# Kernel tuning notes

Measured on AMD Instinct MI355X. Metric: run time of the kernel, lower is better.

## Reference

```python
import jax, jax.numpy as jnp
import numpy as np

EPS = 1e-5

def layer_norm(x, g, b):
    m = jnp.mean(x, axis=-1, keepdims=True)
    v = jnp.mean(jnp.square(x - m), axis=-1, keepdims=True)
    return (x - m) * jax.lax.rsqrt(v + EPS) * g + b

def setup_inputs() -> dict:
    key = jax.random.key(0)
    ks = jax.random.split(key, 12)
    B, N, D, C = 1, 384, 128, 128
    s_in = 1.0 / np.sqrt(D)
    s_c = 1.0 / np.sqrt(C)
    return {
        "z": jax.random.normal(ks[0], (B, N, N, D), dtype=jnp.float32),
        "mask": jnp.ones((B, N, N), dtype=jnp.float32),
        "norm_g": jnp.ones((D,), jnp.float32),
        "norm_b": jnp.zeros((D,), jnp.float32),
        "norm_out_g": jnp.ones((C,), jnp.float32),
        "norm_out_b": jnp.zeros((C,), jnp.float32),
        "Wa": jax.random.normal(ks[1], (D, C), jnp.float32) * s_in,
        "ba": jnp.zeros((C,), jnp.float32),
        "Wb": jax.random.normal(ks[2], (D, C), jnp.float32) * s_in,
        "bb": jnp.zeros((C,), jnp.float32),
        "Wga": jax.random.normal(ks[3], (D, C), jnp.float32) * s_in,
        "bga": jnp.zeros((C,), jnp.float32),
        "Wgb": jax.random.normal(ks[4], (D, C), jnp.float32) * s_in,
        "bgb": jnp.zeros((C,), jnp.float32),
        "Wo": jax.random.normal(ks[5], (C, D), jnp.float32) * s_c,
        "bo": jnp.zeros((D,), jnp.float32),
        "Wgo": jax.random.normal(ks[6], (D, D), jnp.float32) * s_in,
        "bgo": jnp.zeros((D,), jnp.float32),
    }

def reference(z, mask, norm_g, norm_b, norm_out_g, norm_out_b,
              Wa, ba, Wb, bb, Wga, bga, Wgb, bgb, Wo, bo, Wgo, bgo):
    # z: [B,N,N,D]; mask: [B,N,N]
    z_norm = layer_norm(z, norm_g, norm_b)
    left = (z_norm @ Wa + ba) * jax.nn.sigmoid(z_norm @ Wga + bga)   # [B,N,N,C]
    right = (z_norm @ Wb + bb) * jax.nn.sigmoid(z_norm @ Wgb + bgb)  # [B,N,N,C]
    m = mask[..., None]
    left = left * m
    right = right * m
    # z_out[b,i,j,c] = sum_k left[b,i,k,c] * right[b,j,k,c]
    z_out = jnp.einsum('bikc,bjkc->bijc', left, right)
    z_out = layer_norm(z_out, norm_out_g, norm_out_b)
    z_update = (z_out @ Wo + bo) * jax.nn.sigmoid(z_norm @ Wgo + bgo)
    return z_update
```

## Files before the change

kernel.cpp:

```cpp
#include <hip/hip_runtime.h>


#define NSEQ 384
#define NROW (384 * 384)

typedef __attribute__((ext_vector_type(8))) short bf16x8;
typedef __attribute__((ext_vector_type(4))) float f32x4;

__device__ __forceinline__ float sigmoidf_(float x) {
    return 1.0f / (1.0f + __expf(-x));
}
__device__ __forceinline__ unsigned short bf16_rne(float f) {
    unsigned int u = __float_as_uint(f);
    u += 0x7FFFu + ((u >> 16) & 1u);
    return (unsigned short)(u >> 16);
}
__device__ __forceinline__ float bf16_tof(unsigned short h) {
    return __uint_as_float(((unsigned int)h) << 16);
}

__global__ __launch_bounds__(256) void proj_kernel(
    const float* __restrict__ z, const float* __restrict__ mask,
    const float* __restrict__ ng, const float* __restrict__ nb,
    const float* __restrict__ Wa, const float* __restrict__ ba,
    const float* __restrict__ Wga, const float* __restrict__ bga,
    const float* __restrict__ Wb, const float* __restrict__ bb,
    const float* __restrict__ Wgb, const float* __restrict__ bgb,
    const float* __restrict__ Wgo, const float* __restrict__ bgo,
    unsigned short* __restrict__ lH, unsigned short* __restrict__ lL,
    unsigned short* __restrict__ rH, unsigned short* __restrict__ rL,
    float* __restrict__ go)
{
    __shared__ float At[128][68];
    __shared__ float Ws[128][64];
    float* Tt = &Ws[0][0];
    const int t = threadIdx.x;
    const int tx = t & 15, ty = t >> 4;
    const int row0 = blockIdx.x * 64;

#pragma unroll
    for (int it = 0; it < 8; ++it) {
        const int f = t + it * 256;
        const int r = f >> 5;
        const int c4 = (f & 31) << 2;
        const float4 v = *reinterpret_cast<const float4*>(z + (size_t)(row0 + r) * 128 + c4);
        At[c4 + 0][r] = v.x;
        At[c4 + 1][r] = v.y;
        At[c4 + 2][r] = v.z;
        At[c4 + 3][r] = v.w;
    }
    __syncthreads();

    {
        const int r = t >> 2, sub = t & 3;
        float s = 0.f, ss = 0.f;
#pragma unroll
        for (int q = 0; q < 32; ++q) {
            const float x = At[sub * 32 + q][r];
            s += x;
            ss += x * x;
        }
        s += __shfl_xor(s, 1);  ss += __shfl_xor(ss, 1);
        s += __shfl_xor(s, 2);  ss += __shfl_xor(ss, 2);
        const float m = s * (1.f / 128.f);
        const float inv = rsqrtf(ss * (1.f / 128.f) - m * m + 1e-5f);
#pragma unroll
        for (int q = 0; q < 32; ++q) {
            const int k = sub * 32 + q;
            At[k][r] = (At[k][r] - m) * inv * ng[k] + nb[k];
        }
    }

    float mk[4];
#pragma unroll
    for (int m = 0; m < 4; ++m) mk[m] = mask[row0 + ty * 4 + m];

    float accA[4][4], accG[4][4];

#define LOAD_W(Wp, h)                                                              \
    __syncthreads();                                                               \
    _Pragma("unroll")                                                              \
    for (int it = 0; it < 8; ++it) {                                               \
        const int f = t + it * 256;                                                \
        const int k = f >> 4;                                                      \
        const int c4 = (f & 15) << 2;                                              \
        *reinterpret_cast<float4*>(&Ws[k][c4]) =                                   \
            *reinterpret_cast<const float4*>((Wp) + k * 128 + (h) * 64 + c4);      \
    }                                                                              \
    __syncthreads();

#define MM(acc)                                                                    \
    _Pragma("unroll")                                                              \
    for (int m = 0; m < 4; ++m)                                                    \
        _Pragma("unroll")                                                          \
        for (int n = 0; n < 4; ++n) (acc)[m][n] = 0.f;                             \
    _Pragma("unroll 8")                                                            \
    for (int k = 0; k < 128; ++k) {                                                \
        const float4 a = *reinterpret_cast<const float4*>(&At[k][ty * 4]);         \
        const float4 b = *reinterpret_cast<const float4*>(&Ws[k][tx * 4]);         \
        const float av[4] = {a.x, a.y, a.z, a.w};                                  \
        const float bv[4] = {b.x, b.y, b.z, b.w};                                  \
        _Pragma("unroll")                                                          \
        for (int m = 0; m < 4; ++m)                                                \
            _Pragma("unroll")                                                      \
            for (int n = 0; n < 4; ++n) (acc)[m][n] = fmaf(av[m], bv[n], (acc)[m][n]); \
    }

#define STORE_T_BF(dstH, dstL, h, EXPR_X, EXPR_Y, EXPR_Z, EXPR_W)                  \
    __syncthreads();                                  \
    _Pragma("unroll")                                                              \
    for (int m = 0; m < 4; ++m) {                                                  \
        Tt[(tx * 4 + 0) * 65 + ty * 4 + m] = (EXPR_X);                             \
        Tt[(tx * 4 + 1) * 65 + ty * 4 + m] = (EXPR_Y);                             \
        Tt[(tx * 4 + 2) * 65 + ty * 4 + m] = (EXPR_Z);                             \
        Tt[(tx * 4 + 3) * 65 + ty * 4 + m] = (EXPR_W);                             \
    }                                                                              \
    __syncthreads();                                                               \
    _Pragma("unroll")                                                              \
    for (int p = 0; p < 4; ++p) {                                                  \
        const int f = t + p * 256;                                    \
        const int c = f >> 4;                                 \
        const int r4 = (f & 15) << 2;                                              \
        ushort4 hv, lv;                                                            \
        const float v0 = Tt[c * 65 + r4 + 0];                                      \
        const float v1 = Tt[c * 65 + r4 + 1];                                      \
        const float v2 = Tt[c * 65 + r4 + 2];                                      \
        const float v3 = Tt[c * 65 + r4 + 3];                                      \
        hv.x = bf16_rne(v0); lv.x = bf16_rne(v0 - bf16_tof(hv.x));                 \
        hv.y = bf16_rne(v1); lv.y = bf16_rne(v1 - bf16_tof(hv.y));                 \
        hv.z = bf16_rne(v2); lv.z = bf16_rne(v2 - bf16_tof(hv.z));                 \
        hv.w = bf16_rne(v3); lv.w = bf16_rne(v3 - bf16_tof(hv.w));                 \
        const size_t off = (size_t)((h) * 64 + c) * NROW + row0 + r4;              \
        *reinterpret_cast<ushort4*>((dstH) + off) = hv;                            \
        *reinterpret_cast<ushort4*>((dstL) + off) = lv;                            \
    }

    for (int h = 0; h < 2; ++h) {
        const int c0 = h * 64 + tx * 4;

        LOAD_W(Wa, h);  MM(accA);
        LOAD_W(Wga, h); MM(accG);
        {
            const float4 b1 = *reinterpret_cast<const float4*>(ba + c0);
            const float4 b2 = *reinterpret_cast<const float4*>(bga + c0);
            STORE_T_BF(lH, lL, h,
                (accA[m][0] + b1.x) * sigmoidf_(accG[m][0] + b2.x) * mk[m],
                (accA[m][1] + b1.y) * sigmoidf_(accG[m][1] + b2.y) * mk[m],
                (accA[m][2] + b1.z) * sigmoidf_(accG[m][2] + b2.z) * mk[m],
                (accA[m][3] + b1.w) * sigmoidf_(accG[m][3] + b2.w) * mk[m]);
        }

        LOAD_W(Wb, h);  MM(accA);
        LOAD_W(Wgb, h); MM(accG);
        {
            const float4 b1 = *reinterpret_cast<const float4*>(bb + c0);
            const float4 b2 = *reinterpret_cast<const float4*>(bgb + c0);
            STORE_T_BF(rH, rL, h,
                (accA[m][0] + b1.x) * sigmoidf_(accG[m][0] + b2.x) * mk[m],
                (accA[m][1] + b1.y) * sigmoidf_(accG[m][1] + b2.y) * mk[m],
                (accA[m][2] + b1.z) * sigmoidf_(accG[m][2] + b2.z) * mk[m],
                (accA[m][3] + b1.w) * sigmoidf_(accG[m][3] + b2.w) * mk[m]);
        }

        LOAD_W(Wgo, h); MM(accA);
        {
            const float4 b1 = *reinterpret_cast<const float4*>(bgo + c0);
#pragma unroll
            for (int m = 0; m < 4; ++m) {
                float4 o;
                o.x = sigmoidf_(accA[m][0] + b1.x);
                o.y = sigmoidf_(accA[m][1] + b1.y);
                o.z = sigmoidf_(accA[m][2] + b1.z);
                o.w = sigmoidf_(accA[m][3] + b1.w);
                *reinterpret_cast<float4*>(go + (size_t)(row0 + ty * 4 + m) * 128 + c0) = o;
            }
        }
    }
#undef LOAD_W
#undef MM
#undef STORE_T_BF
}

__global__ __launch_bounds__(256) void tri_mfma_kernel(
    const unsigned short* __restrict__ lH, const unsigned short* __restrict__ lL,
    const unsigned short* __restrict__ rH, const unsigned short* __restrict__ rL,
    float* __restrict__ zo)
{
    __shared__ unsigned short Ah[128][40];
    __shared__ unsigned short Al[128][40];
    __shared__ unsigned short Bh[128][40];
    __shared__ unsigned short Bl[128][40];

    const int t = threadIdx.x;
    const int w = t >> 6, l = t & 63;
    const int c  = blockIdx.x;
    const int i0 = blockIdx.y * 128;
    const int j0 = blockIdx.z * 128;
    const int iw = (w >> 1) * 64;
    const int jw = (w & 1) * 64;
    const int lr = l & 15;
    const int lk = (l >> 4) * 8;

    f32x4 acc[4][4];
#pragma unroll
    for (int m = 0; m < 4; ++m)
#pragma unroll
        for (int n = 0; n < 4; ++n) {
            acc[m][n][0] = 0.f; acc[m][n][1] = 0.f;
            acc[m][n][2] = 0.f; acc[m][n][3] = 0.f;
        }

    const size_t cbase = (size_t)c * NROW;

    for (int kc = 0; kc < NSEQ; kc += 32) {
        __syncthreads();
#pragma unroll
        for (int p = 0; p < 2; ++p) {
            const int f = t + p * 256;
            const int row = f >> 2;
            const int seg = (f & 3) * 8;
            const size_t gi = cbase + (size_t)(i0 + row) * NSEQ + kc + seg;
            const size_t gj = cbase + (size_t)(j0 + row) * NSEQ + kc + seg;
            *reinterpret_cast<uint4*>(&Ah[row][seg]) = *reinterpret_cast<const uint4*>(lH + gi);
            *reinterpret_cast<uint4*>(&Al[row][seg]) = *reinterpret_cast<const uint4*>(lL + gi);
            *reinterpret_cast<uint4*>(&Bh[row][seg]) = *reinterpret_cast<const uint4*>(rH + gj);
            *reinterpret_cast<uint4*>(&Bl[row][seg]) = *reinterpret_cast<const uint4*>(rL + gj);
        }
        __syncthreads();

        bf16x8 ah[4], al[4];
#pragma unroll
        for (int m = 0; m < 4; ++m) {
            ah[m] = *reinterpret_cast<const bf16x8*>(&Ah[iw + m * 16 + lr][lk]);
            al[m] = *reinterpret_cast<const bf16x8*>(&Al[iw + m * 16 + lr][lk]);
        }
#pragma unroll
        for (int n = 0; n < 4; ++n) {
            const bf16x8 bh = *reinterpret_cast<const bf16x8*>(&Bh[jw + n * 16 + lr][lk]);
            const bf16x8 bl = *reinterpret_cast<const bf16x8*>(&Bl[jw + n * 16 + lr][lk]);
#pragma unroll
            for (int m = 0; m < 4; ++m) {
                acc[m][n] = __builtin_amdgcn_mfma_f32_16x16x32_bf16(al[m], bh, acc[m][n], 0, 0, 0);
                acc[m][n] = __builtin_amdgcn_mfma_f32_16x16x32_bf16(ah[m], bl, acc[m][n], 0, 0, 0);
                acc[m][n] = __builtin_amdgcn_mfma_f32_16x16x32_bf16(ah[m], bh, acc[m][n], 0, 0, 0);
            }
        }
    }

    float* zp = zo + cbase;
#pragma unroll
    for (int m = 0; m < 4; ++m) {
        const int rb = i0 + iw + m * 16 + (l >> 4) * 4;
#pragma unroll
        for (int n = 0; n < 4; ++n) {
            const int cb = j0 + jw + n * 16 + lr;
#pragma unroll
            for (int r = 0; r < 4; ++r)
                zp[(size_t)(rb + r) * NSEQ + cb] = acc[m][n][r];
        }
    }
}

__global__ __launch_bounds__(256) void out_kernel(
    const float* __restrict__ zo,
    const float* __restrict__ nog, const float* __restrict__ nob,
    const float* __restrict__ Wo, const float* __restrict__ bo,
    const float* __restrict__ go, float* __restrict__ out)
{
    __shared__ float At[128][68];
    __shared__ float Ws[128][64];
    const int t = threadIdx.x;
    const int tx = t & 15, ty = t >> 4;
    const int row0 = blockIdx.x * 64;

#pragma unroll
    for (int it = 0; it < 8; ++it) {
        const int f = t + it * 256;
        const int c = f >> 4;
        const int j4 = (f & 15) << 2;
        const float4 v = *reinterpret_cast<const float4*>(zo + (size_t)c * NROW + row0 + j4);
        *reinterpret_cast<float4*>(&At[c][j4]) = v;
    }
    __syncthreads();

    {
        const int r = t >> 2, sub = t & 3;
        float s = 0.f, ss = 0.f;
#pragma unroll
        for (int q = 0; q < 32; ++q) {
            const float x = At[sub * 32 + q][r];
            s += x;
            ss += x * x;
        }
        s += __shfl_xor(s, 1);  ss += __shfl_xor(ss, 1);
        s += __shfl_xor(s, 2);  ss += __shfl_xor(ss, 2);
        const float m = s * (1.f / 128.f);
        const float inv = rsqrtf(ss * (1.f / 128.f) - m * m + 1e-5f);
#pragma unroll
        for (int q = 0; q < 32; ++q) {
            const int k = sub * 32 + q;
            At[k][r] = (At[k][r] - m) * inv * nog[k] + nob[k];
        }
    }

    float accA[4][4];
    for (int h = 0; h < 2; ++h) {
        const int c0 = h * 64 + tx * 4;
        __syncthreads();
#pragma unroll
        for (int it = 0; it < 8; ++it) {
            const int f = t + it * 256;
            const int k = f >> 4;
            const int c4 = (f & 15) << 2;
            *reinterpret_cast<float4*>(&Ws[k][c4]) =
                *reinterpret_cast<const float4*>(Wo + k * 128 + h * 64 + c4);
        }
        __syncthreads();
#pragma unroll
        for (int m = 0; m < 4; ++m)
#pragma unroll
            for (int n = 0; n < 4; ++n) accA[m][n] = 0.f;
#pragma unroll 8
        for (int k = 0; k < 128; ++k) {
            const float4 a = *reinterpret_cast<const float4*>(&At[k][ty * 4]);
            const float4 b = *reinterpret_cast<const float4*>(&Ws[k][tx * 4]);
            const float av[4] = {a.x, a.y, a.z, a.w};
            const float bv[4] = {b.x, b.y, b.z, b.w};
#pragma unroll
            for (int m = 0; m < 4; ++m)
#pragma unroll
                for (int n = 0; n < 4; ++n) accA[m][n] = fmaf(av[m], bv[n], accA[m][n]);
        }
        const float4 b1 = *reinterpret_cast<const float4*>(bo + c0);
#pragma unroll
        for (int m = 0; m < 4; ++m) {
            const size_t base = (size_t)(row0 + ty * 4 + m) * 128 + c0;
            const float4 g = *reinterpret_cast<const float4*>(go + base);
            float4 o;
            o.x = (accA[m][0] + b1.x) * g.x;
            o.y = (accA[m][1] + b1.y) * g.y;
            o.z = (accA[m][2] + b1.z) * g.z;
            o.w = (accA[m][3] + b1.w) * g.w;
            *reinterpret_cast<float4*>(out + base) = o;
        }
    }
}

extern "C" void kernel_launch(void* const* d_in, const int* in_sizes, int n_in,
                              void* d_out, int out_size, void* d_ws, size_t ws_size,
                              hipStream_t stream)
{
    const float* z    = (const float*)d_in[0];
    const float* mask = (const float*)d_in[1];
    const float* ng   = (const float*)d_in[2];
    const float* nb   = (const float*)d_in[3];
    const float* nog  = (const float*)d_in[4];
    const float* nob  = (const float*)d_in[5];
    const float* Wa   = (const float*)d_in[6];
    const float* ba   = (const float*)d_in[7];
    const float* Wb   = (const float*)d_in[8];
    const float* bb   = (const float*)d_in[9];
    const float* Wga  = (const float*)d_in[10];
    const float* bga  = (const float*)d_in[11];
    const float* Wgb  = (const float*)d_in[12];
    const float* bgb  = (const float*)d_in[13];
    const float* Wo   = (const float*)d_in[14];
    const float* bo   = (const float*)d_in[15];
    const float* Wgo  = (const float*)d_in[16];
    const float* bgo  = (const float*)d_in[17];
    float* outp = (float*)d_out;

    const size_t S = (size_t)NROW * 128;
    float* ws = (float*)d_ws;
    float* go = ws;
    float* zo = ws + S;
    unsigned short* lH = (unsigned short*)(ws + 2 * S);
    unsigned short* lL = lH + S;
    unsigned short* rH = lH + 2 * S;
    unsigned short* rL = lH + 3 * S;

    proj_kernel<<<NROW / 64, 256, 0, stream>>>(z, mask, ng, nb, Wa, ba, Wga, bga,
                                               Wb, bb, Wgb, bgb, Wgo, bgo,
                                               lH, lL, rH, rL, go);
    tri_mfma_kernel<<<dim3(128, 3, 3), 256, 0, stream>>>(lH, lL, rH, rL, zo);
    out_kernel<<<NROW / 64, 256, 0, stream>>>(zo, nog, nob, Wo, bo, go, outp);
}
```

Measured before the change: 656.0 us.

## Move input projections onto bf16x3 MFMA with pre-split transposed weights

The input projection kernel moves from FP32 FMA tiles to split-bf16 (hi/lo, three MFMA products) 16x16x32 matrix instructions. A new prep kernel converts the five weight matrices into transposed hi/lo bf16 copies, stored in the zo workspace that is later overwritten. LayerNorm now runs from registers and writes bf16 hi/lo into LDS instead of a transposed fp32 tile. The aim is to cut the FP32 ALU cost of the five 128x128 GEMMs per row block, at the price of an extra launch and slightly lower precision from dropping the lo*lo term.

```diff
diff --git a/kernel.cpp b/kernel.cpp
--- a/kernel.cpp
+++ b/kernel.cpp
@@ -19,166 +19,185 @@
     return __uint_as_float(((unsigned int)h) << 16);
 }
 
+__global__ void prep_kernel(const float* __restrict__ Wa, const float* __restrict__ Wga,
+                            const float* __restrict__ Wb, const float* __restrict__ Wgb,
+                            const float* __restrict__ Wgo, unsigned short* __restrict__ wt)
+{
+    const int wsel = blockIdx.x;
+    const int n = blockIdx.y;
+    const int k = threadIdx.x;
+    const float* W = (wsel == 0) ? Wa : (wsel == 1) ? Wga : (wsel == 2) ? Wb
+                     : (wsel == 3) ? Wgb : Wgo;
+    const float v = W[k * 128 + n];
+    const unsigned short h = bf16_rne(v);
+    const unsigned short lo = bf16_rne(v - bf16_tof(h));
+    wt[(size_t)((wsel * 2 + 0) * 128 + n) * 128 + k] = h;
+    wt[(size_t)((wsel * 2 + 1) * 128 + n) * 128 + k] = lo;
+}
+
 __global__ __launch_bounds__(256) void proj_kernel(
     const float* __restrict__ z, const float* __restrict__ mask,
     const float* __restrict__ ng, const float* __restrict__ nb,
-    const float* __restrict__ Wa, const float* __restrict__ ba,
-    const float* __restrict__ Wga, const float* __restrict__ bga,
-    const float* __restrict__ Wb, const float* __restrict__ bb,
-    const float* __restrict__ Wgb, const float* __restrict__ bgb,
-    const float* __restrict__ Wgo, const float* __restrict__ bgo,
+    const unsigned short* __restrict__ wt,
+    const float* __restrict__ ba, const float* __restrict__ bga,
+    const float* __restrict__ bb, const float* __restrict__ bgb,
+    const float* __restrict__ bgo,
     unsigned short* __restrict__ lH, unsigned short* __restrict__ lL,
     unsigned short* __restrict__ rH, unsigned short* __restrict__ rL,
     float* __restrict__ go)
 {
-    __shared__ float At[128][68];
-    __shared__ float Ws[128][64];
-    float* Tt = &Ws[0][0];
+    __shared__ unsigned short Zh[4][64][40];
+    __shared__ unsigned short Zl[4][64][40];
+    __shared__ unsigned short Wh[4][64][40];
+    __shared__ unsigned short Wl[4][64][40];
+
     const int t = threadIdx.x;
-    const int tx = t & 15, ty = t >> 4;
+    const int w = t >> 6, l = t & 63;
+    const int lr = l & 15, g = l >> 4;
+    const int lk = g * 8;
     const int row0 = blockIdx.x * 64;
-
-#pragma unroll
-    for (int it = 0; it < 8; ++it) {
-        const int f = t + it * 256;
-        const int r = f >> 5;
-        const int c4 = (f & 31) << 2;
-        const float4 v = *reinterpret_cast<const float4*>(z + (size_t)(row0 + r) * 128 + c4);
-        At[c4 + 0][r] = v.x;
-        At[c4 + 1][r] = v.y;
-        At[c4 + 2][r] = v.z;
-        At[c4 + 3][r] = v.w;
-    }
-    __syncthreads();
 
     {
         const int r = t >> 2, sub = t & 3;
+        float v[32];
+#pragma unroll
+        for (int j = 0; j < 8; ++j) {
+            const float4 x = *reinterpret_cast<const float4*>(
+                z + (size_t)(row0 + r) * 128 + sub * 32 + j * 4);
+            v[j * 4 + 0] = x.x; v[j * 4 + 1] = x.y;
+            v[j * 4 + 2] = x.z; v[j * 4 + 3] = x.w;
+        }
         float s = 0.f, ss = 0.f;
 #pragma unroll
-        for (int q = 0; q < 32; ++q) {
-            const float x = At[sub * 32 + q][r];
-            s += x;
-            ss += x * x;
-        }
+        for (int q = 0; q < 32; ++q) { s += v[q]; ss += v[q] * v[q]; }
         s += __shfl_xor(s, 1);  ss += __shfl_xor(ss, 1);
         s += __shfl_xor(s, 2);  ss += __shfl_xor(ss, 2);
-        const float m = s * (1.f / 128.f);
-        const float inv = rsqrtf(ss * (1.f / 128.f) - m * m + 1e-5f);
+        const float mu = s * (1.f / 128.f);
+        const float inv = rsqrtf(ss * (1.f / 128.f) - mu * mu + 1e-5f);
+        unsigned short hq[32], lq[32];
 #pragma unroll
         for (int q = 0; q < 32; ++q) {
             const int k = sub * 32 + q;
-            At[k][r] = (At[k][r] - m) * inv * ng[k] + nb[k];
-        }
-    }
-
+            const float x = (v[q] - mu) * inv * ng[k] + nb[k];
+            hq[q] = bf16_rne(x);
+            lq[q] = bf16_rne(x - bf16_tof(hq[q]));
+        }
+#pragma unroll
+        for (int j = 0; j < 8; ++j) {
+            ushort4 ph = {hq[j*4+0], hq[j*4+1], hq[j*4+2], hq[j*4+3]};
+            ushort4 pl = {lq[j*4+0], lq[j*4+1], lq[j*4+2], lq[j*4+3]};
+            *reinterpret_cast<ushort4*>(&Zh[sub][r][j * 4]) = ph;
+            *reinterpret_cast<ushort4*>(&Zl[sub][r][j * 4]) = pl;
+        }
+    }
+    __syncthreads();
+
+    bf16x8 ah[4], al[4];
+#pragma unroll
+    for (int kc = 0; kc < 4; ++kc) {
+        ah[kc] = *reinterpret_cast<const bf16x8*>(&Zh[kc][w * 16 + lr][lk]);
+        al[kc] = *reinterpret_cast<const bf16x8*>(&Zl[kc][w * 16 + lr][lk]);
+    }
     float mk[4];
 #pragma unroll
-    for (int m = 0; m < 4; ++m) mk[m] = mask[row0 + ty * 4 + m];
-
-    float accA[4][4], accG[4][4];
-
-#define LOAD_W(Wp, h)                                                              \
+    for (int r4 = 0; r4 < 4; ++r4) mk[r4] = mask[row0 + w * 16 + g * 4 + r4];
+
+    f32x4 accA[4], accG[4];
+
+#define STAGE_W(widx, hh)                                                          \
     __syncthreads();                                                               \
     _Pragma("unroll")                                                              \
-    for (int it = 0; it < 8; ++it) {                                               \
+    for (int it = 0; it < 4; ++it) {                                               \
         const int f = t + it * 256;                                                \
-        const int k = f >> 4;                                                      \
-        const int c4 = (f & 15) << 2;                                              \
-        *reinterpret_cast<float4*>(&Ws[k][c4]) =                                   \
-            *reinterpret_cast<const float4*>((Wp) + k * 128 + (h) * 64 + c4);      \
+        const int n = f >> 4;                                                      \
+        const int k8 = (f & 15) * 8;                                               \
+        const int kc = k8 >> 5, ko = k8 & 31;                                      \
+        *reinterpret_cast<uint4*>(&Wh[kc][n][ko]) = *reinterpret_cast<const uint4*>(  \
+            &wt[(size_t)(((widx) * 2 + 0) * 128 + (hh) * 64 + n) * 128 + k8]);     \
+        *reinterpret_cast<uint4*>(&Wl[kc][n][ko]) = *reinterpret_cast<const uint4*>(  \
+            &wt[(size_t)(((widx) * 2 + 1) * 128 + (hh) * 64 + n) * 128 + k8]);     \
     }                                                                              \
     __syncthreads();
 
-#define MM(acc)                                                                    \
+#define GEMM(acc)                                                                  \
     _Pragma("unroll")                                                              \
-    for (int m = 0; m < 4; ++m)                                                    \
+    for (int nt = 0; nt < 4; ++nt) {                                               \
+        acc[nt][0] = 0.f; acc[nt][1] = 0.f; acc[nt][2] = 0.f; acc[nt][3] = 0.f;    \
+    }                                                                              \
+    _Pragma("unroll")                                                              \
+    for (int kc = 0; kc < 4; ++kc) {                                               \
         _Pragma("unroll")                                                          \
-        for (int n = 0; n < 4; ++n) (acc)[m][n] = 0.f;                             \
-    _Pragma("unroll 8")                                                            \
-    for (int k = 0; k < 128; ++k) {                                                \
-        const float4 a = *reinterpret_cast<const float4*>(&At[k][ty * 4]);         \
-        const float4 b = *reinterpret_cast<const float4*>(&Ws[k][tx * 4]);         \
-        const float av[4] = {a.x, a.y, a.z, a.w};                                  \
-        const float bv[4] = {b.x, b.y, b.z, b.w};                                  \
+        for (int nt = 0; nt < 4; ++nt) {                                           \
+            const bf16x8 bh = *reinterpret_cast<const bf16x8*>(&Wh[kc][nt * 16 + lr][lk]); \
+            const bf16x8 bl = *reinterpret_cast<const bf16x8*>(&Wl[kc][nt * 16 + lr][lk]); \
+            acc[nt] = __builtin_amdgcn_mfma_f32_16x16x32_bf16(al[kc], bh, acc[nt], 0, 0, 0); \
+            acc[nt] = __builtin_amdgcn_mfma_f32_16x16x32_bf16(ah[kc], bl, acc[nt], 0, 0, 0); \
+            acc[nt] = __builtin_amdgcn_mfma_f32_16x16x32_bf16(ah[kc], bh, acc[nt], 0, 0, 0); \
+        }                                                                          \
+    }
+
+#define EPI_PAIR(dstH, dstL, bA, bG, hh)                                           \
+    __syncthreads();                       \
+    {                                                                              \
+        float* Tt = reinterpret_cast<float*>(&Wh[0][0][0]);                        \
         _Pragma("unroll")                                                          \
-        for (int m = 0; m < 4; ++m)                                                \
+        for (int nt = 0; nt < 4; ++nt) {                                           \
+            const int cl = nt * 16 + lr;                                           \
+            const float vbA = (bA)[(hh) * 64 + cl];                                \
+            const float vbG = (bG)[(hh) * 64 + cl];                                \
             _Pragma("unroll")                                                      \
-            for (int n = 0; n < 4; ++n) (acc)[m][n] = fmaf(av[m], bv[n], (acc)[m][n]); \
-    }
-
-#define STORE_T_BF(dstH, dstL, h, EXPR_X, EXPR_Y, EXPR_Z, EXPR_W)                  \
-    __syncthreads();                                  \
-    _Pragma("unroll")                                                              \
-    for (int m = 0; m < 4; ++m) {                                                  \
-        Tt[(tx * 4 + 0) * 65 + ty * 4 + m] = (EXPR_X);                             \
-        Tt[(tx * 4 + 1) * 65 + ty * 4 + m] = (EXPR_Y);                             \
-        Tt[(tx * 4 + 2) * 65 + ty * 4 + m] = (EXPR_Z);                             \
-        Tt[(tx * 4 + 3) * 65 + ty * 4 + m] = (EXPR_W);                             \
-    }                                                                              \
-    __syncthreads();                                                               \
-    _Pragma("unroll")                                                              \
-    for (int p = 0; p < 4; ++p) {                                                  \
-        const int f = t + p * 256;                                    \
-        const int c = f >> 4;                                 \
-        const int r4 = (f & 15) << 2;                                              \
-        ushort4 hv, lv;                                                            \
-        const float v0 = Tt[c * 65 + r4 + 0];                                      \
-        const float v1 = Tt[c * 65 + r4 + 1];                                      \
-        const float v2 = Tt[c * 65 + r4 + 2];                                      \
-        const float v3 = Tt[c * 65 + r4 + 3];                                      \
-        hv.x = bf16_rne(v0); lv.x = bf16_rne(v0 - bf16_tof(hv.x));                 \
-        hv.y = bf16_rne(v1); lv.y = bf16_rne(v1 - bf16_tof(hv.y));                 \
-        hv.z = bf16_rne(v2); lv.z = bf16_rne(v2 - bf16_tof(hv.z));                 \
-        hv.w = bf16_rne(v3); lv.w = bf16_rne(v3 - bf16_tof(hv.w));                 \
-        const size_t off = (size_t)((h) * 64 + c) * NROW + row0 + r4;              \
-        *reinterpret_cast<ushort4*>((dstH) + off) = hv;                            \
-        *reinterpret_cast<ushort4*>((dstL) + off) = lv;                            \
+            for (int r4 = 0; r4 < 4; ++r4) {                                       \
+                const int rowl = w * 16 + g * 4 + r4;                              \
+                Tt[cl * 65 + rowl] =                                               \
+                    (accA[nt][r4] + vbA) * sigmoidf_(accG[nt][r4] + vbG) * mk[r4]; \
+            }                                                                      \
+        }                                                                          \
+        __syncthreads();                                                           \
+        _Pragma("unroll")                                                          \
+        for (int p = 0; p < 4; ++p) {                                              \
+            const int f = t + p * 256;                                             \
+            const int c = f >> 4;                                                  \
+            const int r4b = (f & 15) * 4;                                          \
+            const float v0 = Tt[c * 65 + r4b + 0];                                 \
+            const float v1 = Tt[c * 65 + r4b + 1];                                 \
+            const float v2 = Tt[c * 65 + r4b + 2];                                 \
+            const float v3 = Tt[c * 65 + r4b + 3];                                 \
+            ushort4 hv, lv;                                                        \
+            hv.x = bf16_rne(v0); lv.x = bf16_rne(v0 - bf16_tof(hv.x));             \
+            hv.y = bf16_rne(v1); lv.y = bf16_rne(v1 - bf16_tof(hv.y));             \
+            hv.z = bf16_rne(v2); lv.z = bf16_rne(v2 - bf16_tof(hv.z));             \
+            hv.w = bf16_rne(v3); lv.w = bf16_rne(v3 - bf16_tof(hv.w));             \
+            const size_t off = (size_t)((hh) * 64 + c) * NROW + row0 + r4b;        \
+            *reinterpret_cast<ushort4*>((dstH) + off) = hv;                        \
+            *reinterpret_cast<ushort4*>((dstL) + off) = lv;                        \
+        }                                                                          \
     }
 
     for (int h = 0; h < 2; ++h) {
-        const int c0 = h * 64 + tx * 4;
-
-        LOAD_W(Wa, h);  MM(accA);
-        LOAD_W(Wga, h); MM(accG);
-        {
-            const float4 b1 = *reinterpret_cast<const float4*>(ba + c0);
-            const float4 b2 = *reinterpret_cast<const float4*>(bga + c0);
-            STORE_T_BF(lH, lL, h,
-                (accA[m][0] + b1.x) * sigmoidf_(accG[m][0] + b2.x) * mk[m],
-                (accA[m][1] + b1.y) * sigmoidf_(accG[m][1] + b2.y) * mk[m],
-                (accA[m][2] + b1.z) * sigmoidf_(accG[m][2] + b2.z) * mk[m],
-                (accA[m][3] + b1.w) * sigmoidf_(accG[m][3] + b2.w) * mk[m]);
-        }
-
-        LOAD_W(Wb, h);  MM(accA);
-        LOAD_W(Wgb, h); MM(accG);
-        {
-            const float4 b1 = *reinterpret_cast<const float4*>(bb + c0);
-            const float4 b2 = *reinterpret_cast<const float4*>(bgb + c0);
-            STORE_T_BF(rH, rL, h,
-                (accA[m][0] + b1.x) * sigmoidf_(accG[m][0] + b2.x) * mk[m],
-                (accA[m][1] + b1.y) * sigmoidf_(accG[m][1] + b2.y) * mk[m],
-                (accA[m][2] + b1.z) * sigmoidf_(accG[m][2] + b2.z) * mk[m],
-                (accA[m][3] + b1.w) * sigmoidf_(accG[m][3] + b2.w) * mk[m]);
-        }
-
-        LOAD_W(Wgo, h); MM(accA);
-        {
-            const float4 b1 = *reinterpret_cast<const float4*>(bgo + c0);
-#pragma unroll
-            for (int m = 0; m < 4; ++m) {
-                float4 o;
-                o.x = sigmoidf_(accA[m][0] + b1.x);
-                o.y = sigmoidf_(accA[m][1] + b1.y);
-                o.z = sigmoidf_(accA[m][2] + b1.z);
-                o.w = sigmoidf_(accA[m][3] + b1.w);
-                *reinterpret_cast<float4*>(go + (size_t)(row0 + ty * 4 + m) * 128 + c0) = o;
+        STAGE_W(0, h); GEMM(accA);
+        STAGE_W(1, h); GEMM(accG);
+        EPI_PAIR(lH, lL, ba, bga, h);
+
+        STAGE_W(2, h); GEMM(accA);
+        STAGE_W(3, h); GEMM(accG);
+        EPI_PAIR(rH, rL, bb, bgb, h);
+
+        STAGE_W(4, h); GEMM(accA);
+#pragma unroll
+        for (int nt = 0; nt < 4; ++nt) {
+            const int cl = nt * 16 + lr;
+            const float vb = bgo[h * 64 + cl];
+#pragma unroll
+            for (int r4 = 0; r4 < 4; ++r4) {
+                const int rowl = w * 16 + g * 4 + r4;
+                go[(size_t)(row0 + rowl) * 128 + h * 64 + cl] =
+                    sigmoidf_(accA[nt][r4] + vb);
             }
         }
     }
-#undef LOAD_W
-#undef MM
-#undef STORE_T_BF
+#undef STAGE_W
+#undef GEMM
+#undef EPI_PAIR
 }
 
 __global__ __launch_bounds__(256) void tri_mfma_kernel(
@@ -335,12 +354,12 @@
 #pragma unroll
         for (int m = 0; m < 4; ++m) {
             const size_t base = (size_t)(row0 + ty * 4 + m) * 128 + c0;
-            const float4 g = *reinterpret_cast<const float4*>(go + base);
+            const float4 gv = *reinterpret_cast<const float4*>(go + base);
             float4 o;
-            o.x = (accA[m][0] + b1.x) * g.x;
-            o.y = (accA[m][1] + b1.y) * g.y;
-            o.z = (accA[m][2] + b1.z) * g.z;
-            o.w = (accA[m][3] + b1.w) * g.w;
+            o.x = (accA[m][0] + b1.x) * gv.x;
+            o.y = (accA[m][1] + b1.y) * gv.y;
+            o.z = (accA[m][2] + b1.z) * gv.z;
+            o.w = (accA[m][3] + b1.w) * gv.w;
             *reinterpret_cast<float4*>(out + base) = o;
         }
     }
@@ -374,13 +393,15 @@
     float* ws = (float*)d_ws;
     float* go = ws;
     float* zo = ws + S;
+    unsigned short* wt = (unsigned short*)zo;
     unsigned short* lH = (unsigned short*)(ws + 2 * S);
     unsigned short* lL = lH + S;
     unsigned short* rH = lH + 2 * S;
     unsigned short* rL = lH + 3 * S;
 
-    proj_kernel<<<NROW / 64, 256, 0, stream>>>(z, mask, ng, nb, Wa, ba, Wga, bga,
-                                               Wb, bb, Wgb, bgb, Wgo, bgo,
+    prep_kernel<<<dim3(5, 128), 128, 0, stream>>>(Wa, Wga, Wb, Wgb, Wgo, wt);
+    proj_kernel<<<NROW / 64, 256, 0, stream>>>(z, mask, ng, nb, wt,
+                                               ba, bga, bb, bgb, bgo,
                                                lH, lL, rH, rL, go);
     tri_mfma_kernel<<<dim3(128, 3, 3), 256, 0, stream>>>(lH, lL, rH, rL, zo);
     out_kernel<<<NROW / 64, 256, 0, stream>>>(zo, nog, nob, Wo, bo, go, outp);
```

Measured after the change: 535.4 us. 18.4% less time.
